# Kernel tuning notes

Measured on AMD Instinct MI355X. Metric: run time of the kernel, lower is better.

## Reference

```python
import jax, jax.numpy as jnp
import numpy as np

B, T, D, H = 2, 2048, 1024, 16
HD = D // H


def setup_inputs() -> dict:
    key = jax.random.key(0)
    ks = jax.random.split(key, 5)
    s = 1.0 / np.sqrt(D)
    return {
        "z": jax.random.normal(ks[0], (B, T, D), jnp.float32),
        "w_q": jax.random.normal(ks[1], (D, D), jnp.float32) * s,
        "w_k": jax.random.normal(ks[2], (D, D), jnp.float32) * s,
        "w_v": jax.random.normal(ks[3], (D, D), jnp.float32) * s,
        "w_o": jax.random.normal(ks[4], (D, D), jnp.float32) * s,
    }


def reference(z, w_q, w_k, w_v, w_o):
    # projections: nn.Linear(x) = x @ W.T; weights here stored as [D, D] applied as x @ w
    q = jnp.einsum('btd,de->bte', z, w_q).reshape(B, T, H, HD).transpose(0, 2, 1, 3)  # [B,H,T,hd]
    k = jnp.einsum('btd,de->bte', z, w_k).reshape(B, T, H, HD).transpose(0, 2, 1, 3)
    v = jnp.einsum('btd,de,', z, w_v).reshape(B, T, H, HD).transpose(0, 2, 1, 3) if False else jnp.einsum('btd,de->bte', z, w_v).reshape(B, T, H, HD).transpose(0, 2, 1, 3)
    scale = 1.0 / jnp.sqrt(jnp.float32(HD))
    scores = jnp.einsum('bhqd,bhkd->bhqk', q, k) * scale  # [B,H,T,T]
    causal = jnp.triu(jnp.ones((T, T), bool), k=1)  # True above diagonal -> masked
    scores = jnp.where(causal[None, None], -jnp.inf, scores)
    attn = jax.nn.softmax(scores, axis=-1)
    ctx = jnp.einsum('bhqk,bhkd->bhqd', attn, v)  # [B,H,T,hd]
    ctx = ctx.transpose(0, 2, 1, 3).reshape(B, T, D)
    return jnp.einsum('btd,de->bte', ctx, w_o)
```

## Files before the change

### kernel.cpp

```cpp
#include <hip/hip_runtime.h>
#include <hip/hip_bf16.h>

typedef __hip_bfloat16 bf16;
typedef __attribute__((ext_vector_type(8))) short bf16x8;
typedef __attribute__((ext_vector_type(4))) float f32x4;

#define MFMA16(a, b, c) __builtin_amdgcn_mfma_f32_16x16x32_bf16(a, b, c, 0, 0, 0)

constexpr int Bc = 2, Tc = 2048, Dc = 1024, Hc = 16, HDc = 64;
constexpr int BTc = Bc * Tc;

struct alignas(16) BV8 { bf16 v[8]; };

__global__ __launch_bounds__(256)
void cast_f32_to_bf16(const float* __restrict__ in, bf16* __restrict__ out, int n) {
  int i = (blockIdx.x * 256 + threadIdx.x) * 8;
  if (i >= n) return;
  float4 a = *(const float4*)(in + i);
  float4 b = *(const float4*)(in + i + 4);
  BV8 r;
  r.v[0] = __float2bfloat16(a.x); r.v[1] = __float2bfloat16(a.y);
  r.v[2] = __float2bfloat16(a.z); r.v[3] = __float2bfloat16(a.w);
  r.v[4] = __float2bfloat16(b.x); r.v[5] = __float2bfloat16(b.y);
  r.v[6] = __float2bfloat16(b.z); r.v[7] = __float2bfloat16(b.w);
  *(BV8*)(out + i) = r;
}

__global__ __launch_bounds__(256)
void wT_kernel(const float* __restrict__ w0, const float* __restrict__ w1,
               const float* __restrict__ w2, const float* __restrict__ w3,
               bf16* __restrict__ o0, bf16* __restrict__ o1,
               bf16* __restrict__ o2, bf16* __restrict__ o3) {
  const int which = blockIdx.z;
  const float* src = which == 0 ? w0 : which == 1 ? w1 : which == 2 ? w2 : w3;
  bf16* dst = which == 0 ? o0 : which == 1 ? o1 : which == 2 ? o2 : o3;
  const float scale = (which == 0) ? 0.125f : 1.0f;
  __shared__ float tile[32][33];
  const int tx = threadIdx.x, ty = threadIdx.y;
  const int e0 = blockIdx.x * 32, d0 = blockIdx.y * 32;
#pragma unroll
  for (int rr = 0; rr < 4; ++rr) {
    int r = ty + rr * 8;
    tile[r][tx] = src[(size_t)(d0 + r) * Dc + e0 + tx];
  }
  __syncthreads();
#pragma unroll
  for (int rr = 0; rr < 4; ++rr) {
    int r = ty + rr * 8;
    dst[(size_t)(e0 + r) * Dc + d0 + tx] = __float2bfloat16(tile[tx][r] * scale);
  }
}

__device__ inline void store_c(float* p, float v) { *p = v; }
__device__ inline void store_c(bf16* p, float v) { *p = __float2bfloat16(v); }

template <typename CT>
__global__ __launch_bounds__(256)
void gemm_bt_kernel(const bf16* __restrict__ A, const bf16* __restrict__ Bt,
                    CT* __restrict__ C, int M, int N, int K) {
  __shared__ bf16 As[128 * 32];
  __shared__ bf16 Bs[128 * 32];
  const int t = threadIdx.x;
  const int lane = t & 63, w = t >> 6;
  const int wr = w >> 1, wc = w & 1;
  const int m0 = blockIdx.y * 128, n0 = blockIdx.x * 128;
  const int l15 = lane & 15, l4 = lane >> 4;
  const int srow = lane >> 2;
  const int scol = (lane & 3) * 8;

  f32x4 acc[4][4] = {};

  for (int k0 = 0; k0 < K; k0 += 32) {
#pragma unroll
    for (int j = 0; j < 2; ++j) {
      const int ch = j * 4 + w;
      const int row = ch * 16 + srow;
      __builtin_amdgcn_global_load_lds(
          (const __attribute__((address_space(1))) void*)(A + (size_t)(m0 + row) * K + k0 + scol),
          (__attribute__((address_space(3))) void*)(As + ch * 512), 16, 0, 0);
      __builtin_amdgcn_global_load_lds(
          (const __attribute__((address_space(1))) void*)(Bt + (size_t)(n0 + row) * K + k0 + scol),
          (__attribute__((address_space(3))) void*)(Bs + ch * 512), 16, 0, 0);
    }
    __syncthreads();

    bf16x8 af[4], bg[4];
#pragma unroll
    for (int m = 0; m < 4; ++m)
      af[m] = *(const bf16x8*)(As + (wr * 64 + m * 16 + l15) * 32 + l4 * 8);
#pragma unroll
    for (int n = 0; n < 4; ++n)
      bg[n] = *(const bf16x8*)(Bs + (wc * 64 + n * 16 + l15) * 32 + l4 * 8);
#pragma unroll
    for (int m = 0; m < 4; ++m)
#pragma unroll
      for (int n = 0; n < 4; ++n)
        acc[m][n] = MFMA16(af[m], bg[n], acc[m][n]);
    __syncthreads();
  }

#pragma unroll
  for (int m = 0; m < 4; ++m) {
    const int row = m0 + wr * 64 + m * 16 + l4 * 4;
#pragma unroll
    for (int n = 0; n < 4; ++n) {
      const int col = n0 + wc * 64 + n * 16 + l15;
#pragma unroll
      for (int r = 0; r < 4; ++r)
        store_c(&C[(size_t)(row + r) * N + col], acc[m][n][r]);
    }
  }
}

__global__ __launch_bounds__(256)
void attn_kernel(const bf16* __restrict__ Q, const bf16* __restrict__ Kg, int ldqk,
                 const bf16* __restrict__ Vt, bf16* __restrict__ O) {
  const int t = threadIdx.x;
  const int lane = t & 63, w = t >> 6;
  const int l15 = lane & 15, l4 = lane >> 4;
  const int bh = blockIdx.y, b = bh >> 4, h = bh & 15;
  const int lo = blockIdx.x;
  const int hi = 31 - lo;
  const int qlo = lo * 64 + w * 16;
  const int qhi = hi * 64 + w * 16;
  const int nch = hi + 1;

  __shared__ bf16 Ks[2][64 * 64];
  __shared__ bf16 Vs[2][64 * 64];
  __shared__ bf16 Ph[4][16][72];
  __shared__ bf16 Pl[4][16][72];

  const int srow_in = lane >> 3;
  const int scb = lane & 7;

  const bf16* qph = Q + (size_t)(b * Tc + qhi + l15) * ldqk + h * HDc + l4 * 8;
  const bf16x8 ah0 = *(const bf16x8*)(qph);
  const bf16x8 ah1 = *(const bf16x8*)(qph + 32);
  const bf16* qpl = Q + (size_t)(b * Tc + qlo + l15) * ldqk + h * HDc + l4 * 8;
  const bf16x8 al0 = *(const bf16x8*)(qpl);
  const bf16x8 al1 = *(const bf16x8*)(qpl + 32);

  f32x4 ch[4] = {}, cl[4] = {};
  float shr = 0.0f, slr = 0.0f;

  auto stage = [&](int buf, int c) {
    const int kv0 = c * 64;
#pragma unroll
    for (int i = 0; i < 4; ++i) {
      const int u = w * 4 + i;
      const int ul = u & 7;
      const int row = ul * 8 + srow_in;
      const int cbs = scb ^ (row & 7);
      if (u < 8) {
        const bf16* src = Kg + (size_t)(b * Tc + kv0 + row) * ldqk + h * HDc + cbs * 8;
        __builtin_amdgcn_global_load_lds(
            (const __attribute__((address_space(1))) void*)src,
            (__attribute__((address_space(3))) void*)(Ks[buf] + ul * 512), 16, 0, 0);
      } else {
        const bf16* src = Vt + (size_t)(h * HDc + row) * BTc + b * Tc + kv0 + cbs * 8;
        __builtin_amdgcn_global_load_lds(
            (const __attribute__((address_space(1))) void*)src,
            (__attribute__((address_space(3))) void*)(Vs[buf] + ul * 512), 16, 0, 0);
      }
    }
  };

  auto qk = [&](const bf16* Kbuf, const bf16x8& a0, const bf16x8& a1, f32x4* s) {
#pragma unroll
    for (int n = 0; n < 4; ++n) {
      const int row = n * 16 + l15;
      const bf16* kr = Kbuf + row * 64;
      bf16x8 bk0 = *(const bf16x8*)(kr + ((l4 ^ (row & 7)) << 3));
      bf16x8 bk1 = *(const bf16x8*)(kr + (((4 + l4) ^ (row & 7)) << 3));
      f32x4 zz = {};
      zz = MFMA16(bk0, a0, zz);
      s[n] = MFMA16(bk1, a1, zz);
    }
  };

  auto expP = [&](f32x4* s, bf16 (*Pw)[72], float& srun, int kv0, int qb, bool mask) {
    const int q = qb + l15;
#pragma unroll
    for (int n = 0; n < 4; ++n) {
      float e[4];
#pragma unroll
      for (int r = 0; r < 4; ++r) {
        float v = __expf(s[n][r]);
        if (mask) {
          const int kv = kv0 + n * 16 + l4 * 4 + r;
          v = (kv <= q) ? v : 0.0f;
        }
        e[r] = v;
        srun += v;
      }
      unsigned u0, u1;
      asm("v_cvt_pk_bf16_f32 %0, %1, %2" : "=v"(u0) : "v"(e[0]), "v"(e[1]));
      asm("v_cvt_pk_bf16_f32 %0, %1, %2" : "=v"(u1) : "v"(e[2]), "v"(e[3]));
      uint2 uu; uu.x = u0; uu.y = u1;
      *(uint2*)((char*)(&Pw[l15][0]) + n * 32 + l4 * 8) = uu;
    }
  };

  auto pv = [&](const bf16* Vbuf, bf16 (*Pw)[72], f32x4* ctx) {
    const bf16x8 pa0 = *(const bf16x8*)(&Pw[l15][l4 * 8]);
    const bf16x8 pa1 = *(const bf16x8*)(&Pw[l15][32 + l4 * 8]);
#pragma unroll
    for (int dn = 0; dn < 4; ++dn) {
      const int row = dn * 16 + l15;
      const bf16* vr = Vbuf + row * 64;
      bf16x8 bv0 = *(const bf16x8*)(vr + ((l4 ^ (row & 7)) << 3));
      bf16x8 bv1 = *(const bf16x8*)(vr + (((4 + l4) ^ (row & 7)) << 3));
      ctx[dn] = MFMA16(pa0, bv0, ctx[dn]);
      ctx[dn] = MFMA16(pa1, bv1, ctx[dn]);
    }
  };

  stage(0, 0);
  __syncthreads();

  for (int c = 0; c <= lo; ++c) {
    const int buf = c & 1;
    if (c + 1 < nch) stage(buf ^ 1, c + 1);
    f32x4 sh4[4], sl4[4];
    qk(Ks[buf], ah0, ah1, sh4);
    qk(Ks[buf], al0, al1, sl4);
    expP(sh4, Ph[w], shr, 0, 0, false);
    expP(sl4, Pl[w], slr, c * 64, qlo, c == lo);
    pv(Vs[buf], Ph[w], ch);
    pv(Vs[buf], Pl[w], cl);
    __syncthreads();
  }
  for (int c = lo + 1; c <= hi; ++c) {
    const int buf = c & 1;
    if (c + 1 < nch) stage(buf ^ 1, c + 1);
    f32x4 sh4[4];
    qk(Ks[buf], ah0, ah1, sh4);
    expP(sh4, Ph[w], shr, c * 64, qhi, c == hi);
    pv(Vs[buf], Ph[w], ch);
    __syncthreads();
  }

  shr += __shfl_xor(shr, 16);
  shr += __shfl_xor(shr, 32);
  slr += __shfl_xor(slr, 16);
  slr += __shfl_xor(slr, 32);
  float ihr[4], ilr[4];
#pragma unroll
  for (int r = 0; r < 4; ++r) {
    ihr[r] = 1.0f / __shfl(shr, l4 * 4 + r);
    ilr[r] = 1.0f / __shfl(slr, l4 * 4 + r);
  }
#pragma unroll
  for (int dn = 0; dn < 4; ++dn)
#pragma unroll
    for (int r = 0; r < 4; ++r) {
      O[(size_t)(b * Tc + qhi + l4 * 4 + r) * Dc + h * HDc + dn * 16 + l15] =
          __float2bfloat16(ch[dn][r] * ihr[r]);
      O[(size_t)(b * Tc + qlo + l4 * 4 + r) * Dc + h * HDc + dn * 16 + l15] =
          __float2bfloat16(cl[dn][r] * ilr[r]);
    }
}

extern "C" void kernel_launch(void* const* d_in, const int* in_sizes, int n_in,
                              void* d_out, int out_size, void* d_ws, size_t ws_size,
                              hipStream_t stream) {
  const float* z  = (const float*)d_in[0];
  const float* wq = (const float*)d_in[1];
  const float* wk = (const float*)d_in[2];
  const float* wv = (const float*)d_in[3];
  const float* wo = (const float*)d_in[4];
  float* out = (float*)d_out;

  char* ws = (char*)d_ws;
  const size_t MB = 1ull << 20;
  bf16* zb  = (bf16*)(ws + 0 * MB);
  bf16* wqT = (bf16*)(ws + 8 * MB);
  bf16* wkT = (bf16*)(ws + 10 * MB);
  bf16* wvT = (bf16*)(ws + 12 * MB);
  bf16* woT = (bf16*)(ws + 14 * MB);
  bf16* QK  = (bf16*)(ws + 16 * MB);
  bf16* Vtb = (bf16*)(ws + 32 * MB);
  bf16* Ctx = (bf16*)(ws + 40 * MB);

  cast_f32_to_bf16<<<dim3(2048), dim3(256), 0, stream>>>(z, zb, Bc * Tc * Dc);
  wT_kernel<<<dim3(32, 32, 4), dim3(32, 8), 0, stream>>>(wq, wk, wv, wo, wqT, wkT, wvT, woT);

  gemm_bt_kernel<bf16><<<dim3(16, 32), dim3(256), 0, stream>>>(zb, wqT, QK, 4096, 2048, 1024);
  gemm_bt_kernel<bf16><<<dim3(32, 8), dim3(256), 0, stream>>>(wvT, zb, Vtb, 1024, 4096, 1024);

  attn_kernel<<<dim3(16, 32), dim3(256), 0, stream>>>(QK, QK + 1024, 2048, Vtb, Ctx);

  gemm_bt_kernel<float><<<dim3(8, 32), dim3(256), 0, stream>>>(Ctx, woT, out, 4096, 1024, 1024);
}
```

Measured before the change: 203.8 us.

## Split causal attention KV range across two blocks and combine partial results

Attention work for each paired q-tile block is split along the KV chunk dimension into two halves via blockIdx.z. Each half writes unnormalized bf16 context and row sums, and a new combine kernel adds them and normalizes. This doubles grid parallelism (512 to 1024 blocks) to fill more CUs, at the cost of extra partial-result traffic and a launch. The change also folds log2(e) into the Q weight scale so exp2 replaces expf, adds a swizzled, smaller P buffer in LDS, and sets a launch-bounds occupancy hint. The kernel still uses no running max, and the unnormalized partials are now rounded to bf16 before summing, which adds precision risk.

```diff
diff --git a/kernel.cpp b/kernel.cpp
--- a/kernel.cpp
+++ b/kernel.cpp
@@ -34,7 +34,7 @@
   const int which = blockIdx.z;
   const float* src = which == 0 ? w0 : which == 1 ? w1 : which == 2 ? w2 : w3;
   bf16* dst = which == 0 ? o0 : which == 1 ? o1 : which == 2 ? o2 : o3;
-  const float scale = (which == 0) ? 0.125f : 1.0f;
+  const float scale = (which == 0) ? 0.125f * 1.44269504088896340736f : 1.0f;
   __shared__ float tile[32][33];
   const int tx = threadIdx.x, ty = threadIdx.y;
   const int e0 = blockIdx.x * 32, d0 = blockIdx.y * 32;
@@ -112,23 +112,27 @@
   }
 }
 
-__global__ __launch_bounds__(256)
+__global__ __launch_bounds__(256, 4)
 void attn_kernel(const bf16* __restrict__ Q, const bf16* __restrict__ Kg, int ldqk,
-                 const bf16* __restrict__ Vt, bf16* __restrict__ O) {
+                 const bf16* __restrict__ Vt, bf16* __restrict__ pc0,
+                 bf16* __restrict__ pc1, float* __restrict__ pd0,
+                 float* __restrict__ pd1) {
   const int t = threadIdx.x;
   const int lane = t & 63, w = t >> 6;
   const int l15 = lane & 15, l4 = lane >> 4;
   const int bh = blockIdx.y, b = bh >> 4, h = bh & 15;
-  const int lo = blockIdx.x;
-  const int hi = 31 - lo;
+  const int lo = blockIdx.x, hi = 31 - lo;
+  const int zh = blockIdx.z;
+  const int nch = hi + 1;
+  const int S = (lo >= 8) ? 8 : (16 - lo);
+  const int c0 = zh ? S : 0;
+  const int c1 = zh ? nch : S;
   const int qlo = lo * 64 + w * 16;
   const int qhi = hi * 64 + w * 16;
-  const int nch = hi + 1;
 
   __shared__ bf16 Ks[2][64 * 64];
   __shared__ bf16 Vs[2][64 * 64];
-  __shared__ bf16 Ph[4][16][72];
-  __shared__ bf16 Pl[4][16][72];
+  __shared__ bf16 P[4][16 * 64];
 
   const int srow_in = lane >> 3;
   const int scb = lane & 7;
@@ -142,6 +146,9 @@
 
   f32x4 ch[4] = {}, cl[4] = {};
   float shr = 0.0f, slr = 0.0f;
+
+  char* Pw = (char*)&P[w][0];
+  const int pswz = (l15 & 7) << 4;
 
   auto stage = [&](int buf, int c) {
     const int kv0 = c * 64;
@@ -178,14 +185,14 @@
     }
   };
 
-  auto expP = [&](f32x4* s, bf16 (*Pw)[72], float& srun, int kv0, int qb, bool mask) {
+  auto expP = [&](f32x4* s, float& srun, int kv0, int qb, bool mask) {
     const int q = qb + l15;
 #pragma unroll
     for (int n = 0; n < 4; ++n) {
       float e[4];
 #pragma unroll
       for (int r = 0; r < 4; ++r) {
-        float v = __expf(s[n][r]);
+        float v = __builtin_amdgcn_exp2f(s[n][r]);
         if (mask) {
           const int kv = kv0 + n * 16 + l4 * 4 + r;
           v = (kv <= q) ? v : 0.0f;
@@ -197,13 +204,13 @@
       asm("v_cvt_pk_bf16_f32 %0, %1, %2" : "=v"(u0) : "v"(e[0]), "v"(e[1]));
       asm("v_cvt_pk_bf16_f32 %0, %1, %2" : "=v"(u1) : "v"(e[2]), "v"(e[3]));
       uint2 uu; uu.x = u0; uu.y = u1;
-      *(uint2*)((char*)(&Pw[l15][0]) + n * 32 + l4 * 8) = uu;
+      *(uint2*)(Pw + l15 * 128 + ((n * 32 + l4 * 8) ^ pswz)) = uu;
     }
   };
 
-  auto pv = [&](const bf16* Vbuf, bf16 (*Pw)[72], f32x4* ctx) {
-    const bf16x8 pa0 = *(const bf16x8*)(&Pw[l15][l4 * 8]);
-    const bf16x8 pa1 = *(const bf16x8*)(&Pw[l15][32 + l4 * 8]);
+  auto pv = [&](const bf16* Vbuf, f32x4* ctx) {
+    const bf16x8 pa0 = *(const bf16x8*)(Pw + l15 * 128 + ((l4 * 16) ^ pswz));
+    const bf16x8 pa1 = *(const bf16x8*)(Pw + l15 * 128 + ((64 + l4 * 16) ^ pswz));
 #pragma unroll
     for (int dn = 0; dn < 4; ++dn) {
       const int row = dn * 16 + l15;
@@ -215,50 +222,63 @@
     }
   };
 
-  stage(0, 0);
+  stage(0, c0);
   __syncthreads();
-
-  for (int c = 0; c <= lo; ++c) {
-    const int buf = c & 1;
-    if (c + 1 < nch) stage(buf ^ 1, c + 1);
-    f32x4 sh4[4], sl4[4];
-    qk(Ks[buf], ah0, ah1, sh4);
-    qk(Ks[buf], al0, al1, sl4);
-    expP(sh4, Ph[w], shr, 0, 0, false);
-    expP(sl4, Pl[w], slr, c * 64, qlo, c == lo);
-    pv(Vs[buf], Ph[w], ch);
-    pv(Vs[buf], Pl[w], cl);
+  int par = 0;
+  for (int c = c0; c < c1; ++c) {
+    if (c + 1 < c1) stage(par ^ 1, c + 1);
+    f32x4 s4[4];
+    qk(Ks[par], ah0, ah1, s4);
+    expP(s4, shr, c * 64, qhi, c == hi);
+    pv(Vs[par], ch);
+    if (c <= lo) {
+      qk(Ks[par], al0, al1, s4);
+      expP(s4, slr, c * 64, qlo, c == lo);
+      pv(Vs[par], cl);
+    }
     __syncthreads();
-  }
-  for (int c = lo + 1; c <= hi; ++c) {
-    const int buf = c & 1;
-    if (c + 1 < nch) stage(buf ^ 1, c + 1);
-    f32x4 sh4[4];
-    qk(Ks[buf], ah0, ah1, sh4);
-    expP(sh4, Ph[w], shr, c * 64, qhi, c == hi);
-    pv(Vs[buf], Ph[w], ch);
-    __syncthreads();
-  }
-
-  shr += __shfl_xor(shr, 16);
-  shr += __shfl_xor(shr, 32);
-  slr += __shfl_xor(slr, 16);
-  slr += __shfl_xor(slr, 32);
-  float ihr[4], ilr[4];
-#pragma unroll
-  for (int r = 0; r < 4; ++r) {
-    ihr[r] = 1.0f / __shfl(shr, l4 * 4 + r);
-    ilr[r] = 1.0f / __shfl(slr, l4 * 4 + r);
-  }
+    par ^= 1;
+  }
+
+  shr += __shfl_xor(shr, 16); shr += __shfl_xor(shr, 32);
+  slr += __shfl_xor(slr, 16); slr += __shfl_xor(slr, 32);
+
+  bf16* pco = zh ? pc1 : pc0;
+  float* pdo = zh ? pd1 : pd0;
 #pragma unroll
   for (int dn = 0; dn < 4; ++dn)
 #pragma unroll
     for (int r = 0; r < 4; ++r) {
-      O[(size_t)(b * Tc + qhi + l4 * 4 + r) * Dc + h * HDc + dn * 16 + l15] =
-          __float2bfloat16(ch[dn][r] * ihr[r]);
-      O[(size_t)(b * Tc + qlo + l4 * 4 + r) * Dc + h * HDc + dn * 16 + l15] =
-          __float2bfloat16(cl[dn][r] * ilr[r]);
-    }
+      pco[(size_t)(b * Tc + qhi + l4 * 4 + r) * Dc + h * HDc + dn * 16 + l15] =
+          __float2bfloat16(ch[dn][r]);
+      pco[(size_t)(b * Tc + qlo + l4 * 4 + r) * Dc + h * HDc + dn * 16 + l15] =
+          __float2bfloat16(cl[dn][r]);
+    }
+  if (l4 == 0) {
+    pdo[(size_t)(b * Tc + qhi + l15) * Hc + h] = shr;
+    pdo[(size_t)(b * Tc + qlo + l15) * Hc + h] = slr;
+  }
+}
+
+__global__ __launch_bounds__(256)
+void combine_kernel(const bf16* __restrict__ pcA, const bf16* __restrict__ pcB,
+                    const float* __restrict__ pdA, const float* __restrict__ pdB,
+                    bf16* __restrict__ out) {
+  const int i = blockIdx.x * 256 + threadIdx.x;
+  const int row = i >> 7;
+  const int g = i & 127;
+  const int h = g >> 3;
+  const float invd = 1.0f / (pdA[(size_t)row * Hc + h] + pdB[(size_t)row * Hc + h]);
+  bf16x8 a = *(const bf16x8*)(pcA + (size_t)i * 8);
+  bf16x8 b = *(const bf16x8*)(pcB + (size_t)i * 8);
+  BV8 o;
+#pragma unroll
+  for (int j = 0; j < 8; ++j) {
+    float va = __bfloat162float(((const bf16*)&a)[j]);
+    float vb = __bfloat162float(((const bf16*)&b)[j]);
+    o.v[j] = __float2bfloat16((va + vb) * invd);
+  }
+  *(BV8*)(out + (size_t)i * 8) = o;
 }
 
 extern "C" void kernel_launch(void* const* d_in, const int* in_sizes, int n_in,
@@ -280,7 +300,11 @@
   bf16* woT = (bf16*)(ws + 14 * MB);
   bf16* QK  = (bf16*)(ws + 16 * MB);
   bf16* Vtb = (bf16*)(ws + 32 * MB);
-  bf16* Ctx = (bf16*)(ws + 40 * MB);
+  bf16* pc0 = (bf16*)(ws + 0 * MB);
+  bf16* pc1 = (bf16*)(ws + 40 * MB);
+  float* pd0 = (float*)(ws + 8 * MB);
+  float* pd1 = (float*)(ws + 9 * MB);
+  bf16* Ctx = (bf16*)(ws + 16 * MB);
 
   cast_f32_to_bf16<<<dim3(2048), dim3(256), 0, stream>>>(z, zb, Bc * Tc * Dc);
   wT_kernel<<<dim3(32, 32, 4), dim3(32, 8), 0, stream>>>(wq, wk, wv, wo, wqT, wkT, wvT, woT);
@@ -288,7 +312,9 @@
   gemm_bt_kernel<bf16><<<dim3(16, 32), dim3(256), 0, stream>>>(zb, wqT, QK, 4096, 2048, 1024);
   gemm_bt_kernel<bf16><<<dim3(32, 8), dim3(256), 0, stream>>>(wvT, zb, Vtb, 1024, 4096, 1024);
 
-  attn_kernel<<<dim3(16, 32), dim3(256), 0, stream>>>(QK, QK + 1024, 2048, Vtb, Ctx);
+  attn_kernel<<<dim3(16, 32, 2), dim3(256), 0, stream>>>(QK, QK + 1024, 2048, Vtb,
+                                                         pc0, pc1, pd0, pd1);
+  combine_kernel<<<dim3(2048), dim3(256), 0, stream>>>(pc0, pc1, pd0, pd1, Ctx);
 
   gemm_bt_kernel<float><<<dim3(8, 32), dim3(256), 0, stream>>>(Ctx, woT, out, 4096, 1024, 1024);
 }
```

Measured after the change: 319.3 us. 1.57x slower.
